# Kernel optimization log

Hardware: AMD Instinct MI355X
Metric: run time of the kernel (lower is better)

## Reference

```python
import jax, jax.numpy as jnp
import numpy as np

LOG_STD_MAX = 2.0
LOG_STD_MIN = -5.0
HEIGHT = 4          # tree height -> 16 leaves, 15 internal nodes
TOP_K = 4           # top-k leaves kept in soft gate
SMAX_TEMP = 1.0     # softmax temperature over selected leaf logits


def _path_matrix(height: int) -> np.ndarray:
    """[N_internal, L] matrix with +1 where a leaf's root-to-leaf path goes
    left through a node, -1 where it goes right, 0 otherwise."""
    L = 2 ** height
    P = np.zeros((L - 1, L), dtype=np.float32)
    for leaf in range(L):
        node = 0
        for lvl in range(height):
            bit = (leaf >> (height - 1 - lvl)) & 1
            P[node, leaf] = 1.0 if bit == 0 else -1.0
            node = 2 * node + 1 + bit
    return P


def setup_inputs() -> dict:
    key = jax.random.key(0)
    k0, k1, k2, k3, k4 = jax.random.split(key, 5)
    B, D, A = 262144, 128, 8
    L = 2 ** HEIGHT
    N = L - 1
    x = jax.random.normal(k0, (B, D), dtype=jnp.float32)
    Wn = jax.random.normal(k1, (D, N), dtype=jnp.float32) / np.float32(np.sqrt(D))
    bn = jax.random.normal(k2, (N,), dtype=jnp.float32) * 0.01
    Wl = jax.random.normal(k3, (L, D, 2 * A), dtype=jnp.float32) / np.float32(np.sqrt(D))
    bl = jax.random.normal(k4, (L, 2 * A), dtype=jnp.float32) * 0.01
    return {"x": x, "Wn": Wn, "bn": bn, "Wl": Wl, "bl": bl}


def reference(x, Wn, bn, Wl, bl):
    L = Wl.shape[0]
    P = jnp.asarray(_path_matrix(HEIGHT))              # [N, L] constant

    # --- differentiable-tree routing ---
    node_logits = x @ Wn + bn                          # [B, N]
    leaf_logits = node_logits @ P                      # [B, L]
    vals, idx = jax.lax.top_k(leaf_logits, TOP_K)      # [B, k]
    soft = jax.nn.softmax(vals / SMAX_TEMP, axis=-1)   # [B, k]
    onehot = jax.nn.one_hot(idx, L, dtype=x.dtype)     # [B, k, L]
    gate_soft = jnp.einsum('bk,bkl->bl', soft, onehot) # scatter soft weights
    gate_hard = onehot[:, 0]                           # argmax leaf one-hot
    # hard argmax forward, top-k softmax gradient (straight-through)
    gate = gate_hard + gate_soft - jax.lax.stop_gradient(gate_soft)

    # --- per-leaf linear controllers, gated sum ---
    leaf_out = jnp.einsum('bd,ldo->blo', x, Wl) + bl   # [B, L, 2A]
    out = jnp.einsum('bl,blo->bo', gate, leaf_out)     # [B, 2A]

    A = out.shape[-1] // 2
    mean, log_std = out[:, :A], out[:, A:]
    log_std = jnp.tanh(log_std)
    log_std = LOG_STD_MIN + 0.5 * (LOG_STD_MAX - LOG_STD_MIN) * (log_std + 1.0)
    return mean, log_std
```

## Files before the change

kernel.cpp:

```cpp
#include <hip/hip_runtime.h>
#include <math.h>

#define BLK  256
#define DD   128
#define NN   15
#define NL   16
#define OC   16
#define NLSTR 20
#define MAXT 32
#define TPW  8
#define GAPTHR 1e-3f

typedef __attribute__((ext_vector_type(8))) short short8v;
typedef __attribute__((ext_vector_type(4))) float f32x4;
typedef union { unsigned u[4]; short8v s; } fragu;

__device__ inline unsigned cvt_pk_bf16(float a, float b) {
    unsigned r;
    asm volatile("v_cvt_pk_bf16_f32 %0, %1, %2" : "=v"(r) : "v"(a), "v"(b));
    return r;
}

__device__ inline void split8(const float v[8], short8v& hi, short8v& lo) {
    fragu H, L;
    #pragma unroll
    for (int p = 0; p < 4; ++p) {
        const float a = v[2*p], b = v[2*p+1];
        const unsigned h = cvt_pk_bf16(a, b);
        H.u[p] = h;
        const float ra = a - __uint_as_float(h << 16);
        const float rb = b - __uint_as_float(h & 0xFFFF0000u);
        L.u[p] = cvt_pk_bf16(ra, rb);
    }
    hi = H.s; lo = L.s;
}
__device__ inline short8v pack8hi(const float v[8]) {
    fragu H;
    #pragma unroll
    for (int p = 0; p < 4; ++p) H.u[p] = cvt_pk_bf16(v[2*p], v[2*p+1]);
    return H.s;
}

__global__ __launch_bounds__(BLK, 4)
void dts_fused9(const float* __restrict__ x, const float* __restrict__ Wn,
                const float* __restrict__ bn, const float* __restrict__ Wl,
                const float* __restrict__ bl, float* __restrict__ out, int B)
{
    __shared__ __align__(16) float sNLw[4][64 * NLSTR];
    __shared__ float sBn[NN];
    __shared__ __align__(16) float sBl[NL * OC];
    __shared__ int sPerm[BLK + 16];
    __shared__ int sBins[NL];
    __shared__ int sStarts[NL];
    __shared__ int sTleaf[MAXT];
    __shared__ int sTm0[MAXT];
    __shared__ int sTend[MAXT];
    __shared__ int sNT;

    const int t    = threadIdx.x;
    const int wv   = t >> 6;
    const int lane = t & 63;
    const int lo16 = t & 15;
    const int grp  = (t >> 4) & 3;
    const int rowBase = blockIdx.x * BLK;

    if (t < NN) sBn[t] = bn[t];
    for (int i = t; i < NL * OC; i += BLK) sBl[i] = bl[i];
    if (t < NL) sBins[t] = 0;
    if (t < 16) sPerm[BLK + t] = 0;
    __syncthreads();

    const int waveRow0 = rowBase + wv * 64;
    f32x4 accn[4];
    #pragma unroll
    for (int i = 0; i < 4; ++i) accn[i] = (f32x4){0.f, 0.f, 0.f, 0.f};

    #pragma unroll 1
    for (int c = 0; c < 4; ++c) {
        float bvv[8];
        #pragma unroll
        for (int j = 0; j < 8; ++j) {
            const int k = c * 32 + grp * 8 + j;
            bvv[j] = (lo16 < NN) ? Wn[k * NN + lo16] : 0.f;
        }
        short8v bh, bw;
        split8(bvv, bh, bw);

        #pragma unroll
        for (int i = 0; i < 4; ++i) {
            const float* ap = x + (size_t)(waveRow0 + i * 16 + lo16) * DD + c * 32 + grp * 8;
            const float4 a0 = *(const float4*)ap;
            const float4 a1 = *(const float4*)(ap + 4);
            float av[8];
            av[0]=a0.x; av[1]=a0.y; av[2]=a0.z; av[3]=a0.w;
            av[4]=a1.x; av[5]=a1.y; av[6]=a1.z; av[7]=a1.w;
            short8v ah, al;
            split8(av, ah, al);
            accn[i] = __builtin_amdgcn_mfma_f32_16x16x32_bf16(ah, bh, accn[i], 0, 0, 0);
            accn[i] = __builtin_amdgcn_mfma_f32_16x16x32_bf16(al, bh, accn[i], 0, 0, 0);
            accn[i] = __builtin_amdgcn_mfma_f32_16x16x32_bf16(ah, bw, accn[i], 0, 0, 0);
        }
    }

    float* patch = &sNLw[wv][0];
    #pragma unroll
    for (int i = 0; i < 4; ++i)
        #pragma unroll
        for (int j = 0; j < 4; ++j)
            patch[(i * 16 + grp * 4 + j) * NLSTR + lo16] = accn[i][j];
    asm volatile("s_waitcnt lgkmcnt(0)" ::: "memory");
    __builtin_amdgcn_sched_barrier(0);

    float nl[16];
    {
        const float4* np = (const float4*)&patch[lane * NLSTR];
        const float4 n0 = np[0], n1 = np[1], n2 = np[2], n3 = np[3];
        nl[0]=n0.x; nl[1]=n0.y; nl[2]=n0.z;  nl[3]=n0.w;
        nl[4]=n1.x; nl[5]=n1.y; nl[6]=n1.z;  nl[7]=n1.w;
        nl[8]=n2.x; nl[9]=n2.y; nl[10]=n2.z; nl[11]=n2.w;
        nl[12]=n3.x; nl[13]=n3.y; nl[14]=n3.z;
    }
    #pragma unroll
    for (int n = 0; n < NN; ++n) nl[n] += sBn[n];

    float L2a[4], L3a[8], L4a[16];
    #define EXPAND(src) { \
        float p = src[0], m = -src[0]; \
        L2a[0] = p + src[1]; L2a[1] = p - src[1]; \
        L2a[2] = m + src[2]; L2a[3] = m - src[2]; \
        _Pragma("unroll") \
        for (int i = 0; i < 4; ++i) { L3a[2*i] = L2a[i] + src[3+i]; L3a[2*i+1] = L2a[i] - src[3+i]; } \
        _Pragma("unroll") \
        for (int i = 0; i < 8; ++i) { L4a[2*i] = L3a[i] + src[7+i]; L4a[2*i+1] = L3a[i] - src[7+i]; } }
    EXPAND(nl)
    int best = 0; float bv = L4a[0], sv = -1e30f;
    #pragma unroll
    for (int l = 1; l < NL; ++l) {
        if (L4a[l] > bv) { sv = bv; bv = L4a[l]; best = l; }
        else if (L4a[l] > sv) sv = L4a[l];
    }

    if (bv - sv < GAPTHR) {
        float e[NN];
        #pragma unroll
        for (int n = 0; n < NN; ++n) e[n] = 0.f;
        const float* xrow = x + (size_t)(rowBase + t) * DD;
        for (int d = 0; d < DD; ++d) {
            const float xd = xrow[d];
            const float* wr = Wn + d * NN;
            #pragma unroll
            for (int n = 0; n < NN; ++n) e[n] = fmaf(xd, wr[n], e[n]);
        }
        #pragma unroll
        for (int n = 0; n < NN; ++n) e[n] += sBn[n];
        EXPAND(e)
        best = 0; bv = L4a[0];
        #pragma unroll
        for (int l = 1; l < NL; ++l) if (L4a[l] > bv) { bv = L4a[l]; best = l; }
    }
    #undef EXPAND

    const int rank = atomicAdd(&sBins[best], 1);
    __syncthreads();
    if (t == 0) {
        int s = 0, nt = 0;
        #pragma unroll
        for (int l = 0; l < NL; ++l) {
            sStarts[l] = s;
            const int cn = sBins[l];
            for (int m0 = s; m0 < s + cn; m0 += 16) {
                sTleaf[nt] = l; sTm0[nt] = m0; sTend[nt] = s + cn; ++nt;
            }
            s += cn;
        }
        sNT = nt;
    }
    __syncthreads();
    sPerm[sStarts[best] + rank] = t;
    __syncthreads();
    const int nT = sNT;

    int tleaf[TPW], tm0[TPW], prow[TPW];
    #pragma unroll
    for (int i = 0; i < TPW; ++i) {
        const int tid = wv + i * 4;
        const bool vld = tid < nT;
        tleaf[i] = vld ? sTleaf[tid] : 0;
        tm0[i]   = vld ? sTm0[tid]   : 0;
        prow[i]  = sPerm[tm0[i] + lo16];
    }
    f32x4 accm[TPW];
    #pragma unroll
    for (int i = 0; i < TPW; ++i) accm[i] = (f32x4){0.f, 0.f, 0.f, 0.f};

    #pragma unroll 1
    for (int c = 0; c < 4; ++c) {
        #pragma unroll
        for (int i = 0; i < TPW; ++i) {
            if (wv + i * 4 < nT) {
                const float* ap = x + (size_t)(rowBase + prow[i]) * DD + c * 32 + grp * 8;
                const float4 a0 = *(const float4*)ap;
                const float4 a1 = *(const float4*)(ap + 4);
                float av[8];
                av[0]=a0.x; av[1]=a0.y; av[2]=a0.z; av[3]=a0.w;
                av[4]=a1.x; av[5]=a1.y; av[6]=a1.z; av[7]=a1.w;
                const short8v ah = pack8hi(av);
                const float* bp = Wl + (size_t)tleaf[i] * (DD * OC)
                                     + (size_t)(c * 32 + grp * 8) * OC + lo16;
                float bv2[8];
                #pragma unroll
                for (int j = 0; j < 8; ++j) bv2[j] = bp[j * 16];
                const short8v bh2 = pack8hi(bv2);
                accm[i] = __builtin_amdgcn_mfma_f32_16x16x32_bf16(ah, bh2, accm[i], 0, 0, 0);
            }
        }
    }

    #pragma unroll
    for (int i = 0; i < TPW; ++i) {
        const int tid = wv + i * 4;
        if (tid < nT) {
            const float bias = sBl[tleaf[i] * OC + lo16];
            const int tend = sTend[tid];
            #pragma unroll
            for (int j = 0; j < 4; ++j) {
                const int sl = tm0[i] + grp * 4 + j;
                if (sl < tend) {
                    const int r = sPerm[sl];
                    const size_t grow = (size_t)rowBase + r;
                    const float v = accm[i][j] + bias;
                    if (lo16 < 8) {
                        out[grow * 8 + lo16] = v;
                    } else {
                        out[(size_t)B * 8 + grow * 8 + (lo16 - 8)] =
                            -1.5f + 3.5f * (1.f - 2.f / (__expf(2.f * v) + 1.f));
                    }
                }
            }
        }
    }
}

extern "C" void kernel_launch(void* const* d_in, const int* in_sizes, int n_in,
                              void* d_out, int out_size, void* d_ws, size_t ws_size,
                              hipStream_t stream)
{
    const float* x  = (const float*)d_in[0];
    const float* Wn = (const float*)d_in[1];
    const float* bn = (const float*)d_in[2];
    const float* Wl = (const float*)d_in[3];
    const float* bl = (const float*)d_in[4];
    float* out = (float*)d_out;

    const int B = in_sizes[0] / DD;
    const int blocks = (B + BLK - 1) / BLK;

    hipLaunchKernelGGL(dts_fused9, dim3(blocks), dim3(BLK), 0, stream,
                       x, Wn, bn, Wl, bl, out, B);
}
```

Before: 72.01 us.

## Pre-pack weights into bf16 MFMA fragments and stage outputs for coalesced stores

```diff
diff --git a/kernel.cpp b/kernel.cpp
--- a/kernel.cpp
+++ b/kernel.cpp
@@ -6,7 +6,7 @@
 #define NN   15
 #define NL   16
 #define OC   16
-#define NLSTR 20
+#define OSTR 20
 #define MAXT 32
 #define TPW  8
 #define GAPTHR 1e-3f
@@ -15,12 +15,15 @@
 typedef __attribute__((ext_vector_type(4))) float f32x4;
 typedef union { unsigned u[4]; short8v s; } fragu;
 
+__device__ inline unsigned bf16_rne_u(float f) {
+    unsigned u = __float_as_uint(f);
+    return (u + 0x7FFFu + ((u >> 16) & 1u)) >> 16;
+}
 __device__ inline unsigned cvt_pk_bf16(float a, float b) {
     unsigned r;
     asm volatile("v_cvt_pk_bf16_f32 %0, %1, %2" : "=v"(r) : "v"(a), "v"(b));
     return r;
 }
-
 __device__ inline void split8(const float v[8], short8v& hi, short8v& lo) {
     fragu H, L;
     #pragma unroll
@@ -41,15 +44,40 @@
     return H.s;
 }
 
+__global__ __launch_bounds__(256)
+void dts_prep(const float* __restrict__ Wn, const float* __restrict__ Wl,
+              unsigned short* __restrict__ wlB,
+              unsigned short* __restrict__ wnHi, unsigned short* __restrict__ wnLo)
+{
+    const int id = blockIdx.x * 256 + threadIdx.x;
+    if (id < 32768) {
+        const int j = id & 7, n = (id >> 3) & 15, g = (id >> 7) & 3,
+                  c = (id >> 9) & 3, leaf = id >> 11;
+        const int k = c * 32 + g * 8 + j;
+        wlB[id] = (unsigned short)bf16_rne_u(Wl[((size_t)leaf * DD + k) * OC + n]);
+    } else if (id < 32768 + 2048) {
+        const int id2 = id - 32768;
+        const int j = id2 & 7, n = (id2 >> 3) & 15, g = (id2 >> 7) & 3, c = id2 >> 9;
+        const int k = c * 32 + g * 8 + j;
+        const float v = (n < NN) ? Wn[k * NN + n] : 0.f;
+        const unsigned hb = bf16_rne_u(v);
+        wnHi[id2] = (unsigned short)hb;
+        wnLo[id2] = (unsigned short)bf16_rne_u(v - __uint_as_float(hb << 16));
+    }
+}
+
 __global__ __launch_bounds__(BLK, 4)
-void dts_fused9(const float* __restrict__ x, const float* __restrict__ Wn,
-                const float* __restrict__ bn, const float* __restrict__ Wl,
-                const float* __restrict__ bl, float* __restrict__ out, int B)
+void dts_fused10(const float* __restrict__ x, const float* __restrict__ Wn,
+                 const float* __restrict__ bn, const float* __restrict__ bl,
+                 const unsigned short* __restrict__ wlB,
+                 const unsigned short* __restrict__ wnHi,
+                 const unsigned short* __restrict__ wnLo,
+                 float* __restrict__ out, int B)
 {
-    __shared__ __align__(16) float sNLw[4][64 * NLSTR];
+    __shared__ __align__(16) float sXch[BLK * OSTR];
     __shared__ float sBn[NN];
     __shared__ __align__(16) float sBl[NL * OC];
-    __shared__ int sPerm[BLK + 16];
+    __shared__ int sPerm[BLK];
     __shared__ int sBins[NL];
     __shared__ int sStarts[NL];
     __shared__ int sTleaf[MAXT];
@@ -67,7 +95,6 @@
     if (t < NN) sBn[t] = bn[t];
     for (int i = t; i < NL * OC; i += BLK) sBl[i] = bl[i];
     if (t < NL) sBins[t] = 0;
-    if (t < 16) sPerm[BLK + t] = 0;
     __syncthreads();
 
     const int waveRow0 = rowBase + wv * 64;
@@ -77,15 +104,8 @@
 
     #pragma unroll 1
     for (int c = 0; c < 4; ++c) {
-        float bvv[8];
-        #pragma unroll
-        for (int j = 0; j < 8; ++j) {
-            const int k = c * 32 + grp * 8 + j;
-            bvv[j] = (lo16 < NN) ? Wn[k * NN + lo16] : 0.f;
-        }
-        short8v bh, bw;
-        split8(bvv, bh, bw);
-
+        const short8v bh = *(const short8v*)&wnHi[(c * 64 + lane) * 8];
+        const short8v bw = *(const short8v*)&wnLo[(c * 64 + lane) * 8];
         #pragma unroll
         for (int i = 0; i < 4; ++i) {
             const float* ap = x + (size_t)(waveRow0 + i * 16 + lo16) * DD + c * 32 + grp * 8;
@@ -102,18 +122,20 @@
         }
     }
 
-    float* patch = &sNLw[wv][0];
-    #pragma unroll
-    for (int i = 0; i < 4; ++i)
-        #pragma unroll
-        for (int j = 0; j < 4; ++j)
-            patch[(i * 16 + grp * 4 + j) * NLSTR + lo16] = accn[i][j];
+    {
+        float* patch = &sXch[wv * 64 * OSTR];
+        #pragma unroll
+        for (int i = 0; i < 4; ++i)
+            #pragma unroll
+            for (int j = 0; j < 4; ++j)
+                patch[(i * 16 + grp * 4 + j) * OSTR + lo16] = accn[i][j];
+    }
     asm volatile("s_waitcnt lgkmcnt(0)" ::: "memory");
     __builtin_amdgcn_sched_barrier(0);
 
     float nl[16];
     {
-        const float4* np = (const float4*)&patch[lane * NLSTR];
+        const float4* np = (const float4*)&sXch[t * OSTR];
         const float4 n0 = np[0], n1 = np[1], n2 = np[2], n3 = np[3];
         nl[0]=n0.x; nl[1]=n0.y; nl[2]=n0.z;  nl[3]=n0.w;
         nl[4]=n1.x; nl[5]=n1.y; nl[6]=n1.z;  nl[7]=n1.w;
@@ -180,13 +202,14 @@
     __syncthreads();
     const int nT = sNT;
 
-    int tleaf[TPW], tm0[TPW], prow[TPW];
+    int tleaf[TPW], tm0[TPW], tend[TPW], prow[TPW];
     #pragma unroll
     for (int i = 0; i < TPW; ++i) {
         const int tid = wv + i * 4;
         const bool vld = tid < nT;
         tleaf[i] = vld ? sTleaf[tid] : 0;
         tm0[i]   = vld ? sTm0[tid]   : 0;
+        tend[i]  = vld ? sTend[tid]  : 0;
         prow[i]  = sPerm[tm0[i] + lo16];
     }
     f32x4 accm[TPW];
@@ -205,39 +228,44 @@
                 av[0]=a0.x; av[1]=a0.y; av[2]=a0.z; av[3]=a0.w;
                 av[4]=a1.x; av[5]=a1.y; av[6]=a1.z; av[7]=a1.w;
                 const short8v ah = pack8hi(av);
-                const float* bp = Wl + (size_t)tleaf[i] * (DD * OC)
-                                     + (size_t)(c * 32 + grp * 8) * OC + lo16;
-                float bv2[8];
-                #pragma unroll
-                for (int j = 0; j < 8; ++j) bv2[j] = bp[j * 16];
-                const short8v bh2 = pack8hi(bv2);
-                accm[i] = __builtin_amdgcn_mfma_f32_16x16x32_bf16(ah, bh2, accm[i], 0, 0, 0);
+                const short8v bf = *(const short8v*)&wlB[tleaf[i] * 2048 + (c * 64 + lane) * 8];
+                accm[i] = __builtin_amdgcn_mfma_f32_16x16x32_bf16(ah, bf, accm[i], 0, 0, 0);
             }
         }
     }
 
+    __syncthreads();
     #pragma unroll
     for (int i = 0; i < TPW; ++i) {
-        const int tid = wv + i * 4;
-        if (tid < nT) {
+        if (wv + i * 4 < nT) {
             const float bias = sBl[tleaf[i] * OC + lo16];
-            const int tend = sTend[tid];
             #pragma unroll
             for (int j = 0; j < 4; ++j) {
                 const int sl = tm0[i] + grp * 4 + j;
-                if (sl < tend) {
-                    const int r = sPerm[sl];
-                    const size_t grow = (size_t)rowBase + r;
-                    const float v = accm[i][j] + bias;
-                    if (lo16 < 8) {
-                        out[grow * 8 + lo16] = v;
-                    } else {
-                        out[(size_t)B * 8 + grow * 8 + (lo16 - 8)] =
-                            -1.5f + 3.5f * (1.f - 2.f / (__expf(2.f * v) + 1.f));
-                    }
-                }
+                if (sl < tend[i]) sXch[sPerm[sl] * OSTR + lo16] = accm[i][j] + bias;
             }
         }
+    }
+    __syncthreads();
+    {
+        const float* so = &sXch[t * OSTR];
+        const float4 m0 = *(const float4*)(so);
+        const float4 m1 = *(const float4*)(so + 4);
+        const float4 s0 = *(const float4*)(so + 8);
+        const float4 s1 = *(const float4*)(so + 12);
+
+        const size_t ob = (size_t)(rowBase + t) * 8;
+        *reinterpret_cast<float4*>(&out[ob])     = m0;
+        *reinterpret_cast<float4*>(&out[ob + 4]) = m1;
+
+        float4 r0, r1;
+        #define SQ(v) (-1.5f + 3.5f * (1.f - 2.f / (__expf(2.f * (v)) + 1.f)))
+        r0.x = SQ(s0.x); r0.y = SQ(s0.y); r0.z = SQ(s0.z); r0.w = SQ(s0.w);
+        r1.x = SQ(s1.x); r1.y = SQ(s1.y); r1.z = SQ(s1.z); r1.w = SQ(s1.w);
+        #undef SQ
+        const size_t ob2 = (size_t)B * 8 + ob;
+        *reinterpret_cast<float4*>(&out[ob2])     = r0;
+        *reinterpret_cast<float4*>(&out[ob2 + 4]) = r1;
     }
 }
 
@@ -252,9 +280,14 @@
     const float* bl = (const float*)d_in[4];
     float* out = (float*)d_out;
 
+    unsigned short* wlB  = (unsigned short*)d_ws;
+    unsigned short* wnHi = wlB + 32768;
+    unsigned short* wnLo = wnHi + 2048;
+
     const int B = in_sizes[0] / DD;
     const int blocks = (B + BLK - 1) / BLK;
 
-    hipLaunchKernelGGL(dts_fused9, dim3(blocks), dim3(BLK), 0, stream,
-                       x, Wn, bn, Wl, bl, out, B);
-}
+    hipLaunchKernelGGL(dts_prep, dim3(136), dim3(256), 0, stream, Wn, Wl, wlB, wnHi, wnLo);
+    hipLaunchKernelGGL(dts_fused10, dim3(blocks), dim3(BLK), 0, stream,
+                       x, Wn, bn, bl, wlB, wnHi, wnLo, out, B);
+}
```

Result: slower. 74.33 us (+3.2%).
